# Kernel tuning notes

Hardware: AMD Instinct MI355X
Metric: run time of the kernel (lower is better)

The kernel has to match this reference:

```python
import jax, jax.numpy as jnp
import numpy as np

B, L, D = 2, 2048, 2048
H, KVH = 16, 4
DK = D // H            # 128
REP = H // KVH         # 4
CAP = 50.0


def _rope(x):
    # x: [B, h, L, DK]; rotate-half style RoPE matching the torch module
    half = DK // 2
    inv_freq = 1.0 / (10000.0 ** (jnp.arange(0, DK, 2, dtype=jnp.float32) / DK))
    pos = jnp.arange(x.shape[2], dtype=jnp.float32)
    freqs = pos[:, None] * inv_freq[None, :]          # [L, DK/2]
    cos = jnp.cos(freqs).astype(x.dtype)
    sin = jnp.sin(freqs).astype(x.dtype)
    x1, x2 = x[..., :half], x[..., half:]
    return jnp.concatenate([x1 * cos - x2 * sin, x1 * sin + x2 * cos], axis=-1)


def setup_inputs() -> dict:
    key = jax.random.key(0)
    ks = jax.random.split(key, 7)
    query = jax.random.normal(ks[0], (B, L, D), jnp.float32)
    key_t = jax.random.normal(ks[1], (B, L, D), jnp.float32)
    value = jax.random.normal(ks[2], (B, L, D), jnp.float32)
    mask = jnp.tril(jnp.ones((L, L), dtype=bool))[None, None]  # causal, broadcast over B,H
    s = 1.0 / np.sqrt(D)
    Wq = jax.random.normal(ks[3], (D, D), jnp.float32) * s
    Wk = jax.random.normal(ks[4], (D // REP, D), jnp.float32) * s
    Wv = jax.random.normal(ks[5], (D // REP, D), jnp.float32) * s
    Wo = jax.random.normal(ks[6], (D, D), jnp.float32) * s
    return {"query": query, "key_t": key_t, "value": value, "mask": mask,
            "Wq": Wq, "Wk": Wk, "Wv": Wv, "Wo": Wo}


def reference(query, key_t, value, mask, Wq, Wk, Wv, Wo):
    Lk = key_t.shape[1]
    Q = (query @ Wq.T).reshape(B, L, H, DK).transpose(0, 2, 1, 3)        # [B,H,L,DK]
    K = (key_t @ Wk.T).reshape(B, Lk, KVH, DK).transpose(0, 2, 1, 3)     # [B,KVH,Lk,DK]
    V = (value @ Wv.T).reshape(B, Lk, KVH, DK).transpose(0, 2, 1, 3)
    # repeat_interleave KV heads to match query heads (GQA)
    K = jnp.repeat(K, REP, axis=1)
    V = jnp.repeat(V, REP, axis=1)
    Q = _rope(Q)
    K = _rope(K)
    # module implements "softcap" as a clamp on q/k pre-SDPA
    Q = jnp.clip(Q, -CAP, CAP)
    K = jnp.clip(K, -CAP, CAP)
    scale = 1.0 / np.sqrt(DK)  # SDPA default scaling
    logits = jnp.einsum('bhld,bhkd->bhlk', Q, K) * scale
    neg = jnp.finfo(logits.dtype).min
    logits = logits + jnp.where(mask, jnp.zeros((), logits.dtype), neg)
    attn = jax.nn.softmax(logits, axis=-1)
    out = jnp.einsum('bhlk,bhkd->bhld', attn, V)                         # [B,H,L,DK]
    out = out.transpose(0, 2, 1, 3).reshape(B, L, D)
    return out @ Wo.T
```

## Files before the change

### kernel.cpp

```cpp
#include <hip/hip_runtime.h>

typedef __bf16 bf16;
typedef __bf16 bf16x8 __attribute__((ext_vector_type(8)));
typedef float  f32x4  __attribute__((ext_vector_type(4)));

#define MFMA16(a, b, c) __builtin_amdgcn_mfma_f32_16x16x32_bf16((a), (b), (c), 0, 0, 0)

__device__ inline void gl_lds16(const bf16* g, bf16* l) {
  __builtin_amdgcn_global_load_lds(
      (const __attribute__((address_space(1))) void*)g,
      (__attribute__((address_space(3))) void*)l, 16, 0, 0);
}

__device__ inline bf16x8 cvt8(const float* __restrict__ f) {
  float4 a = *(const float4*)f;
  float4 b = *(const float4*)(f + 4);
  bf16x8 r;
  r[0] = (bf16)a.x; r[1] = (bf16)a.y; r[2] = (bf16)a.z; r[3] = (bf16)a.w;
  r[4] = (bf16)b.x; r[5] = (bf16)b.y; r[6] = (bf16)b.z; r[7] = (bf16)b.w;
  return r;
}

__global__ void cvt_f32_bf16(const float* __restrict__ src, bf16* __restrict__ dst,
                             int n8) {
  int i = blockIdx.x * 256 + threadIdx.x;
  if (i >= n8) return;
  *(bf16x8*)(dst + (size_t)i * 8) = cvt8(src + (size_t)i * 8);
}

__global__ __launch_bounds__(512, 2) void gemm_qkv256(const bf16* __restrict__ qA,
                                                      const bf16* __restrict__ kA,
                                                      const bf16* __restrict__ vA,
                                                      const bf16* __restrict__ W,
                                                      bf16* __restrict__ Qb,
                                                      bf16* __restrict__ Kb,
                                                      bf16* __restrict__ Vb) {
  __shared__ alignas(16) bf16 As[2][32 * 512];
  __shared__ alignas(16) bf16 Bs[2][32 * 512];

  const int tid  = threadIdx.x;
  const int wave = tid >> 6, lane = tid & 63;
  const int wm = wave >> 2, wn = wave & 3;
  const int lr = lane & 15, quad = lane >> 4;
  const int n0 = blockIdx.x * 256, m0 = blockIdx.y * 256;
  const int NS = 32;

  const int range = (n0 < 2048) ? 0 : (n0 < 2560) ? 1 : 2;
  const bf16* Ab = (range == 0) ? qA : (range == 1) ? kA : vA;

  f32x4 vzero = {0.f, 0.f, 0.f, 0.f};
  f32x4 acc[8][4];
#pragma unroll
  for (int mt = 0; mt < 8; ++mt)
#pragma unroll
    for (int nt = 0; nt < 4; ++nt) acc[mt][nt] = vzero;

#define STAGE256(bufi, kk)                                                      \
  do {                                                                          \
    _Pragma("unroll") for (int j = 0; j < 4; ++j) {                             \
      int c = wave * 4 + j;                                                     \
      int mi = c >> 1, sl = c & 1;                                              \
      gl_lds16(Ab + (size_t)(m0 + mi * 16 + lr) * 2048 + (kk) + sl * 32 + quad * 8, \
               &As[bufi][c * 512]);                                             \
      gl_lds16(W + (size_t)(n0 + mi * 16 + lr) * 2048 + (kk) + sl * 32 + quad * 8,  \
               &Bs[bufi][c * 512]);                                             \
    }                                                                           \
  } while (0)

  STAGE256(0, 0);
  int cur = 0;
  for (int t = 0; t < NS; ++t) {
    if (t + 1 < NS) {
      STAGE256(cur ^ 1, (t + 1) * 64);
      asm volatile("s_waitcnt vmcnt(8)" ::: "memory");
    } else {
      asm volatile("s_waitcnt vmcnt(0)" ::: "memory");
    }
    __builtin_amdgcn_s_barrier();

    const bf16* as = As[cur];
    const bf16* bs = Bs[cur];
    bf16x8 af[4], bf0[4], bf1[4];

#pragma unroll
    for (int nt = 0; nt < 4; ++nt)
      bf0[nt] = *(const bf16x8*)(bs + ((wn * 4 + nt) * 2 + 0) * 512 + lane * 8);
#pragma unroll
    for (int mt = 0; mt < 4; ++mt)
      af[mt] = *(const bf16x8*)(as + ((wm * 8 + mt) * 2 + 0) * 512 + lane * 8);
    __builtin_amdgcn_s_setprio(1);
#pragma unroll
    for (int mt = 0; mt < 4; ++mt)
#pragma unroll
      for (int nt = 0; nt < 4; ++nt)
        acc[mt][nt] = MFMA16(af[mt], bf0[nt], acc[mt][nt]);
    __builtin_amdgcn_s_setprio(0);

#pragma unroll
    for (int mt = 0; mt < 4; ++mt)
      af[mt] = *(const bf16x8*)(as + ((wm * 8 + 4 + mt) * 2 + 0) * 512 + lane * 8);
    __builtin_amdgcn_s_setprio(1);
#pragma unroll
    for (int mt = 0; mt < 4; ++mt)
#pragma unroll
      for (int nt = 0; nt < 4; ++nt)
        acc[4 + mt][nt] = MFMA16(af[mt], bf0[nt], acc[4 + mt][nt]);
    __builtin_amdgcn_s_setprio(0);

#pragma unroll
    for (int nt = 0; nt < 4; ++nt)
      bf1[nt] = *(const bf16x8*)(bs + ((wn * 4 + nt) * 2 + 1) * 512 + lane * 8);
#pragma unroll
    for (int mt = 0; mt < 4; ++mt)
      af[mt] = *(const bf16x8*)(as + ((wm * 8 + mt) * 2 + 1) * 512 + lane * 8);
    __builtin_amdgcn_s_setprio(1);
#pragma unroll
    for (int mt = 0; mt < 4; ++mt)
#pragma unroll
      for (int nt = 0; nt < 4; ++nt)
        acc[mt][nt] = MFMA16(af[mt], bf1[nt], acc[mt][nt]);
    __builtin_amdgcn_s_setprio(0);

#pragma unroll
    for (int mt = 0; mt < 4; ++mt)
      af[mt] = *(const bf16x8*)(as + ((wm * 8 + 4 + mt) * 2 + 1) * 512 + lane * 8);
    __builtin_amdgcn_s_setprio(1);
#pragma unroll
    for (int mt = 0; mt < 4; ++mt)
#pragma unroll
      for (int nt = 0; nt < 4; ++nt)
        acc[4 + mt][nt] = MFMA16(af[mt], bf1[nt], acc[4 + mt][nt]);
    __builtin_amdgcn_s_setprio(0);

    __builtin_amdgcn_s_barrier();
    cur ^= 1;
  }
#undef STAGE256

  bf16* Cb = (range == 0) ? Qb : (range == 1) ? Kb : Vb;
  const int ld = (range == 0) ? 2048 : 512;
  const int nb = (range == 0) ? n0 : (range == 1) ? n0 - 2048 : n0 - 2560;
#pragma unroll
  for (int mt = 0; mt < 8; ++mt) {
    int row = m0 + wm * 128 + mt * 16 + quad * 4;
#pragma unroll
    for (int nt = 0; nt < 4; ++nt) {
      int col = nb + wn * 64 + nt * 16 + lr;
#pragma unroll
      for (int e = 0; e < 4; ++e)
        Cb[(size_t)(row + e) * ld + col] = (bf16)acc[mt][nt][e];
    }
  }
}

template <bool OUTF32>
__global__ __launch_bounds__(256) void gemm_bt(const bf16* __restrict__ Ap,
                                               const bf16* __restrict__ W,
                                               void* __restrict__ C0,
                                               int ld0, int M, int N, int K) {
  __shared__ alignas(16) bf16 As[2][16 * 512];
  __shared__ alignas(16) bf16 Bs[2][16 * 512];

  const int tid  = threadIdx.x;
  const int wave = tid >> 6, lane = tid & 63;
  const int wm = wave >> 1, wn = wave & 1;
  const int lr = lane & 15, quad = lane >> 4;
  const int m0 = blockIdx.y * 128, n0 = blockIdx.x * 128;
  const int NS = K >> 6;

  f32x4 vzero = {0.f, 0.f, 0.f, 0.f};
  f32x4 acc[4][4];
#pragma unroll
  for (int mt = 0; mt < 4; ++mt)
#pragma unroll
    for (int nt = 0; nt < 4; ++nt) acc[mt][nt] = vzero;

#define STAGE8(bufi, kk)                                                        \
  do {                                                                          \
    _Pragma("unroll") for (int j = 0; j < 4; ++j) {                             \
      int c = wave * 4 + j;                                                     \
      gl_lds16(W + (size_t)(n0 + (c >> 1) * 16 + lr) * K + (kk) +               \
                   (c & 1) * 32 + quad * 8,                                     \
               &Bs[bufi][c * 512]);                                             \
      gl_lds16(Ap + (size_t)(m0 + (c >> 1) * 16 + lr) * K + (kk) +              \
                   (c & 1) * 32 + quad * 8,                                     \
               &As[bufi][c * 512]);                                             \
    }                                                                           \
  } while (0)

  STAGE8(0, 0);
  int cur = 0;
  for (int t = 0; t < NS; ++t) {
    if (t + 1 < NS) {
      STAGE8(cur ^ 1, (t + 1) * 64);
      asm volatile("s_waitcnt vmcnt(8)" ::: "memory");
    } else {
      asm volatile("s_waitcnt vmcnt(0)" ::: "memory");
    }
    __builtin_amdgcn_s_barrier();
#pragma unroll
    for (int s = 0; s < 2; ++s) {
      bf16x8 af[4], bfg[4];
#pragma unroll
      for (int mt = 0; mt < 4; ++mt)
        af[mt] = *(const bf16x8*)(&As[cur][((wm * 4 + mt) * 2 + s) * 512] + lane * 8);
#pragma unroll
      for (int nt = 0; nt < 4; ++nt)
        bfg[nt] = *(const bf16x8*)(&Bs[cur][((wn * 4 + nt) * 2 + s) * 512] + lane * 8);
      __builtin_amdgcn_s_setprio(1);
#pragma unroll
      for (int mt = 0; mt < 4; ++mt)
#pragma unroll
        for (int nt = 0; nt < 4; ++nt)
          acc[mt][nt] = MFMA16(af[mt], bfg[nt], acc[mt][nt]);
      __builtin_amdgcn_s_setprio(0);
    }
    __builtin_amdgcn_s_barrier();
    cur ^= 1;
  }
#undef STAGE8

#pragma unroll
  for (int mt = 0; mt < 4; ++mt) {
    int row = m0 + wm * 64 + mt * 16 + quad * 4;
#pragma unroll
    for (int nt = 0; nt < 4; ++nt) {
      int col = n0 + wn * 64 + nt * 16 + lr;
#pragma unroll
      for (int e = 0; e < 4; ++e) {
        if (OUTF32)
          ((float*)C0)[(size_t)(row + e) * ld0 + col] = acc[mt][nt][e];
        else
          ((bf16*)C0)[(size_t)(row + e) * ld0 + col] = (bf16)acc[mt][nt][e];
      }
    }
  }
}

__global__ void rope_clip(bf16* __restrict__ X, int heads, float scl) {
  int tpr = heads * 8;
  int idx = blockIdx.x * 256 + threadIdx.x;
  if (idx >= 4096 * tpr) return;
  int r = idx / tpr;
  int rem = idx - r * tpr;
  int h = rem >> 3, j0 = (rem & 7) * 8;
  int l = r & 2047;
  size_t base = (size_t)r * (heads * 128) + h * 128 + j0;
  bf16x8 x1 = *(const bf16x8*)(X + base);
  bf16x8 x2 = *(const bf16x8*)(X + base + 64);
  bf16x8 y1, y2;
#pragma unroll
  for (int t = 0; t < 8; ++t) {
    int j = j0 + t;
    float inv = expf(-(float)j * (9.210340371976184f / 64.0f));
    float s, c;
    sincosf((float)l * inv, &s, &c);
    float a = (float)x1[t], b = (float)x2[t];
    float u = a * c - b * s;
    float v = a * s + b * c;
    y1[t] = (bf16)(fminf(fmaxf(u, -50.f), 50.f) * scl);
    y2[t] = (bf16)(fminf(fmaxf(v, -50.f), 50.f) * scl);
  }
  *(bf16x8*)(X + base)      = y1;
  *(bf16x8*)(X + base + 64) = y2;
}

__global__ void transpose_bf16(const bf16* __restrict__ in, bf16* __restrict__ out,
                               int R, int Cc) {
  __shared__ bf16 t[32][33];
  int b = blockIdx.z;
  const bf16* ip = in + (size_t)b * R * Cc;
  bf16* op = out + (size_t)b * R * Cc;
  int c0 = blockIdx.x * 32, r0 = blockIdx.y * 32;
  int lx = threadIdx.x, ly = threadIdx.y;
#pragma unroll
  for (int i = 0; i < 32; i += 8)
    t[ly + i][lx] = ip[(size_t)(r0 + ly + i) * Cc + c0 + lx];
  __syncthreads();
#pragma unroll
  for (int i = 0; i < 32; i += 8)
    op[(size_t)(c0 + ly + i) * R + r0 + lx] = t[lx][ly + i];
}

__global__ __launch_bounds__(512, 2) void flash(const bf16* __restrict__ Q,
                                                const bf16* __restrict__ Kp,
                                                const bf16* __restrict__ Vt,
                                                bf16* __restrict__ Ctx) {
  __shared__ alignas(16) bf16 Ks[2][16 * 512];
  __shared__ alignas(16) bf16 Vs[2][16 * 512];
  __shared__ alignas(16) bf16 Ps[8][32 * 72];

  const int tid  = threadIdx.x;
  const int wave = tid >> 6, lane = tid & 63;
  const int lr = lane & 15, quad = lane >> 4;
  const int bh = blockIdx.y;
  const int b = bh >> 4, h = bh & 15, hk = h >> 2;
  const int p = blockIdx.x;
  const int qA0 = p * 128, qB0 = (15 - p) * 128;
  const int qbA = qA0 + wave * 16;
  const int qbB = qB0 + wave * 16;
  const int nt = (qB0 + 128) >> 6;

  bf16x8 qfA[4], qfB[4];
  {
    const bf16* qa = Q + ((size_t)(b * 2048 + qbA + lr)) * 2048 + h * 128 + quad * 8;
    const bf16* qbp = Q + ((size_t)(b * 2048 + qbB + lr)) * 2048 + h * 128 + quad * 8;
#pragma unroll
    for (int ks = 0; ks < 4; ++ks) {
      qfA[ks] = *(const bf16x8*)(qa + ks * 32);
      qfB[ks] = *(const bf16x8*)(qbp + ks * 32);
    }
  }

  f32x4 vzero = {0.f, 0.f, 0.f, 0.f};
  f32x4 oA[8], oB[8];
#pragma unroll
  for (int dt = 0; dt < 8; ++dt) { oA[dt] = vzero; oB[dt] = vzero; }
  float flsA[4] = {0.f, 0.f, 0.f, 0.f};
  float flsB[4] = {0.f, 0.f, 0.f, 0.f};

  const bf16* kbase = Kp + (size_t)(b * 2048) * 512 + hk * 128;
  const bf16* vbase = Vt + ((size_t)(b * 512 + hk * 128)) * 2048;

#define STAGE(bufi, kk)                                                         \
  do {                                                                          \
    _Pragma("unroll") for (int j = 0; j < 4; ++j) {                             \
      int c = wave * 4 + j;                                                     \
      if (c < 16) {                                                             \
        gl_lds16(kbase + (size_t)((kk) + (c >> 2) * 16 + lr) * 512 +            \
                     (c & 3) * 32 + quad * 8,                                   \
                 &Ks[bufi][c * 512]);                                           \
      } else {                                                                  \
        int c2 = c - 16;                                                        \
        gl_lds16(vbase + (size_t)((c2 >> 1) * 16 + lr) * 2048 + (kk) +          \
                     (c2 & 1) * 32 + quad * 8,                                  \
                 &Vs[bufi][c2 * 512]);                                          \
      }                                                                         \
    }                                                                           \
  } while (0)

  STAGE(0, 0);
  int cur = 0;

  for (int t = 0; t < nt; ++t) {
    const int k0 = t * 64;
    if (t + 1 < nt) {
      STAGE(cur ^ 1, k0 + 64);
      asm volatile("s_waitcnt vmcnt(4)" ::: "memory");
    } else {
      asm volatile("s_waitcnt vmcnt(0)" ::: "memory");
    }
    __builtin_amdgcn_s_barrier();

    const bf16* ksb = Ks[cur];
    const bf16* vsb = Vs[cur];

    if (k0 <= qbA + 15) {
      f32x4 sA[4], sB[4];
#pragma unroll
      for (int kt = 0; kt < 4; ++kt) { sA[kt] = vzero; sB[kt] = vzero; }
#pragma unroll
      for (int ks = 0; ks < 4; ++ks) {
#pragma unroll
        for (int kt = 0; kt < 4; ++kt) {
          bf16x8 kf = *(const bf16x8*)(ksb + (kt * 4 + ks) * 512 + lane * 8);
          sA[kt] = MFMA16(qfA[ks], kf, sA[kt]);
          sB[kt] = MFMA16(qfB[ks], kf, sB[kt]);
        }
      }
      bf16* pwA = Ps[wave];
      bf16* pwB = Ps[wave] + 16 * 72;
#pragma unroll
      for (int kt = 0; kt < 4; ++kt) {
        int kid = k0 + kt * 16 + lr;
#pragma unroll
        for (int e = 0; e < 4; ++e) {
          int qr = quad * 4 + e;
          float pa = (kid <= qbA + qr) ? __expf(sA[kt][e]) : 0.f;
          float pb = __expf(sB[kt][e]);
          flsA[e] += pa;
          flsB[e] += pb;
          pwA[qr * 72 + kt * 16 + lr] = (bf16)pa;
          pwB[qr * 72 + kt * 16 + lr] = (bf16)pb;
        }
      }
#pragma unroll
      for (int ks2 = 0; ks2 < 2; ++ks2) {
        bf16x8 pfA = *(const bf16x8*)(pwA + (size_t)lr * 72 + ks2 * 32 + quad * 8);
        bf16x8 pfB = *(const bf16x8*)(pwB + (size_t)lr * 72 + ks2 * 32 + quad * 8);
#pragma unroll
        for (int dt = 0; dt < 8; ++dt) {
          bf16x8 vf = *(const bf16x8*)(vsb + (dt * 2 + ks2) * 512 + lane * 8);
          oA[dt] = MFMA16(pfA, vf, oA[dt]);
          oB[dt] = MFMA16(pfB, vf, oB[dt]);
        }
      }
    } else if (k0 <= qbB + 15) {
      f32x4 s[4];
#pragma unroll
      for (int kt = 0; kt < 4; ++kt) s[kt] = vzero;
#pragma unroll
      for (int ks = 0; ks < 4; ++ks) {
#pragma unroll
        for (int kt = 0; kt < 4; ++kt) {
          bf16x8 kf = *(const bf16x8*)(ksb + (kt * 4 + ks) * 512 + lane * 8);
          s[kt] = MFMA16(qfB[ks], kf, s[kt]);
        }
      }
      bf16* pwB = Ps[wave] + 16 * 72;
#pragma unroll
      for (int kt = 0; kt < 4; ++kt) {
        int kid = k0 + kt * 16 + lr;
#pragma unroll
        for (int e = 0; e < 4; ++e) {
          int qr = quad * 4 + e;
          float pb = (kid <= qbB + qr) ? __expf(s[kt][e]) : 0.f;
          flsB[e] += pb;
          pwB[qr * 72 + kt * 16 + lr] = (bf16)pb;
        }
      }
#pragma unroll
      for (int ks2 = 0; ks2 < 2; ++ks2) {
        bf16x8 pf = *(const bf16x8*)(pwB + (size_t)lr * 72 + ks2 * 32 + quad * 8);
#pragma unroll
        for (int dt = 0; dt < 8; ++dt) {
          bf16x8 vf = *(const bf16x8*)(vsb + (dt * 2 + ks2) * 512 + lane * 8);
          oB[dt] = MFMA16(pf, vf, oB[dt]);
        }
      }
    }
    __builtin_amdgcn_s_barrier();
    cur ^= 1;
  }
#undef STAGE

#pragma unroll
  for (int e = 0; e < 4; ++e) {
    float sa = flsA[e];
    sa += __shfl_xor(sa, 1);
    sa += __shfl_xor(sa, 2);
    sa += __shfl_xor(sa, 4);
    sa += __shfl_xor(sa, 8);
    flsA[e] = 1.0f / sa;
    float sb = flsB[e];
    sb += __shfl_xor(sb, 1);
    sb += __shfl_xor(sb, 2);
    sb += __shfl_xor(sb, 4);
    sb += __shfl_xor(sb, 8);
    flsB[e] = 1.0f / sb;
  }

  bf16* ca = Ctx + ((size_t)(b * 2048 + qbA + quad * 4)) * 2048 + h * 128 + lr;
  bf16* cb = Ctx + ((size_t)(b * 2048 + qbB + quad * 4)) * 2048 + h * 128 + lr;
#pragma unroll
  for (int dt = 0; dt < 8; ++dt)
#pragma unroll
    for (int e = 0; e < 4; ++e) {
      ca[(size_t)e * 2048 + dt * 16] = (bf16)(oA[dt][e] * flsA[e]);
      cb[(size_t)e * 2048 + dt * 16] = (bf16)(oB[dt][e] * flsB[e]);
    }
}

extern "C" void kernel_launch(void* const* d_in, const int* in_sizes, int n_in,
                              void* d_out, int out_size, void* d_ws, size_t ws_size,
                              hipStream_t stream) {
  (void)in_sizes; (void)n_in; (void)out_size; (void)ws_size;
  const float* query = (const float*)d_in[0];
  const float* key_t = (const float*)d_in[1];
  const float* value = (const float*)d_in[2];
  const float* Wq = (const float*)d_in[4];
  const float* Wk = (const float*)d_in[5];
  const float* Wv = (const float*)d_in[6];
  const float* Wo = (const float*)d_in[7];

  const size_t MB = 1024ull * 1024ull;
  char* ws  = (char*)d_ws;
  bf16* qbf = (bf16*)(ws);
  bf16* wqb = (bf16*)(ws + 16 * MB);
  bf16* wkb = (bf16*)(ws + 24 * MB);
  bf16* wvb = (bf16*)(ws + 26 * MB);
  bf16* wob = (bf16*)(ws + 28 * MB);
  bf16* Qb  = (bf16*)(ws + 36 * MB);
  bf16* Kb  = (bf16*)(ws + 52 * MB);
  bf16* Vb  = (bf16*)(ws + 56 * MB);
  bf16* Vtb = (bf16*)(ws + 60 * MB);
  bf16* kb16 = (bf16*)(ws + 64 * MB);
  bf16* vb16 = (bf16*)(ws + 80 * MB);
  bf16* Ctx = qbf;

  cvt_f32_bf16<<<4096, 256, 0, stream>>>(query, qbf, 1048576);
  cvt_f32_bf16<<<4096, 256, 0, stream>>>(key_t, kb16, 1048576);
  cvt_f32_bf16<<<4096, 256, 0, stream>>>(value, vb16, 1048576);
  cvt_f32_bf16<<<2048, 256, 0, stream>>>(Wq, wqb, 524288);
  cvt_f32_bf16<<<512, 256, 0, stream>>>(Wk, wkb, 131072);
  cvt_f32_bf16<<<512, 256, 0, stream>>>(Wv, wvb, 131072);
  cvt_f32_bf16<<<2048, 256, 0, stream>>>(Wo, wob, 524288);

  gemm_qkv256<<<dim3(12, 16), 512, 0, stream>>>(qbf, kb16, vb16, wqb, Qb, Kb, Vb);

  rope_clip<<<2048, 256, 0, stream>>>(Qb, 16, 0.08838834764831845f);
  rope_clip<<<512, 256, 0, stream>>>(Kb, 4, 1.0f);

  transpose_bf16<<<dim3(16, 64, 2), dim3(32, 8), 0, stream>>>(Vb, Vtb, 2048, 512);

  flash<<<dim3(8, 32), 512, 0, stream>>>(Qb, Kb, Vtb, Ctx);

  gemm_bt<true><<<dim3(16, 32), 256, 0, stream>>>(
      Ctx, wob, (float*)d_out, 2048, 4096, 2048, 2048);
}
```

Before: 431.5 us.

## Use 256x256 split-K GEMM for output projection with separate reduction

```diff
diff --git a/kernel.cpp b/kernel.cpp
--- a/kernel.cpp
+++ b/kernel.cpp
@@ -28,13 +28,26 @@
   *(bf16x8*)(dst + (size_t)i * 8) = cvt8(src + (size_t)i * 8);
 }
 
-__global__ __launch_bounds__(512, 2) void gemm_qkv256(const bf16* __restrict__ qA,
-                                                      const bf16* __restrict__ kA,
-                                                      const bf16* __restrict__ vA,
-                                                      const bf16* __restrict__ W,
-                                                      bf16* __restrict__ Qb,
-                                                      bf16* __restrict__ Kb,
-                                                      bf16* __restrict__ Vb) {
+__global__ void add_f32(float* __restrict__ dst, const float* __restrict__ src,
+                        int n4) {
+  int i = blockIdx.x * 256 + threadIdx.x;
+  if (i >= n4) return;
+  float4 a = ((const float4*)dst)[i];
+  float4 b = ((const float4*)src)[i];
+  a.x += b.x; a.y += b.y; a.z += b.z; a.w += b.w;
+  ((float4*)dst)[i] = a;
+}
+
+template <int OUTM>
+__global__ __launch_bounds__(512, 2) void gemm256(const bf16* __restrict__ qA,
+                                                  const bf16* __restrict__ kA,
+                                                  const bf16* __restrict__ vA,
+                                                  const bf16* __restrict__ W,
+                                                  bf16* __restrict__ Qb,
+                                                  bf16* __restrict__ Kb,
+                                                  bf16* __restrict__ Vb,
+                                                  float* __restrict__ P0,
+                                                  float* __restrict__ P1) {
   __shared__ alignas(16) bf16 As[2][32 * 512];
   __shared__ alignas(16) bf16 Bs[2][32 * 512];
 
@@ -43,10 +56,17 @@
   const int wm = wave >> 2, wn = wave & 3;
   const int lr = lane & 15, quad = lane >> 4;
   const int n0 = blockIdx.x * 256, m0 = blockIdx.y * 256;
-  const int NS = 32;
-
-  const int range = (n0 < 2048) ? 0 : (n0 < 2560) ? 1 : 2;
-  const bf16* Ab = (range == 0) ? qA : (range == 1) ? kA : vA;
+  const int NS = (OUTM == 0) ? 32 : 16;
+  const int kbase = (OUTM == 0) ? 0 : blockIdx.z * 1024;
+
+  int range = 0;
+  const bf16* Ab;
+  if (OUTM == 0) {
+    range = (n0 < 2048) ? 0 : (n0 < 2560) ? 1 : 2;
+    Ab = (range == 0) ? qA : (range == 1) ? kA : vA;
+  } else {
+    Ab = qA;
+  }
 
   f32x4 vzero = {0.f, 0.f, 0.f, 0.f};
   f32x4 acc[8][4];
@@ -67,11 +87,11 @@
     }                                                                           \
   } while (0)
 
-  STAGE256(0, 0);
+  STAGE256(0, kbase);
   int cur = 0;
   for (int t = 0; t < NS; ++t) {
     if (t + 1 < NS) {
-      STAGE256(cur ^ 1, (t + 1) * 64);
+      STAGE256(cur ^ 1, kbase + (t + 1) * 64);
       asm volatile("s_waitcnt vmcnt(8)" ::: "memory");
     } else {
       asm volatile("s_waitcnt vmcnt(0)" ::: "memory");
@@ -137,101 +157,32 @@
   }
 #undef STAGE256
 
-  bf16* Cb = (range == 0) ? Qb : (range == 1) ? Kb : Vb;
-  const int ld = (range == 0) ? 2048 : 512;
-  const int nb = (range == 0) ? n0 : (range == 1) ? n0 - 2048 : n0 - 2560;
-#pragma unroll
-  for (int mt = 0; mt < 8; ++mt) {
-    int row = m0 + wm * 128 + mt * 16 + quad * 4;
-#pragma unroll
-    for (int nt = 0; nt < 4; ++nt) {
-      int col = nb + wn * 64 + nt * 16 + lr;
-#pragma unroll
-      for (int e = 0; e < 4; ++e)
-        Cb[(size_t)(row + e) * ld + col] = (bf16)acc[mt][nt][e];
-    }
-  }
-}
-
-template <bool OUTF32>
-__global__ __launch_bounds__(256) void gemm_bt(const bf16* __restrict__ Ap,
-                                               const bf16* __restrict__ W,
-                                               void* __restrict__ C0,
-                                               int ld0, int M, int N, int K) {
-  __shared__ alignas(16) bf16 As[2][16 * 512];
-  __shared__ alignas(16) bf16 Bs[2][16 * 512];
-
-  const int tid  = threadIdx.x;
-  const int wave = tid >> 6, lane = tid & 63;
-  const int wm = wave >> 1, wn = wave & 1;
-  const int lr = lane & 15, quad = lane >> 4;
-  const int m0 = blockIdx.y * 128, n0 = blockIdx.x * 128;
-  const int NS = K >> 6;
-
-  f32x4 vzero = {0.f, 0.f, 0.f, 0.f};
-  f32x4 acc[4][4];
-#pragma unroll
-  for (int mt = 0; mt < 4; ++mt)
-#pragma unroll
-    for (int nt = 0; nt < 4; ++nt) acc[mt][nt] = vzero;
-
-#define STAGE8(bufi, kk)                                                        \
-  do {                                                                          \
-    _Pragma("unroll") for (int j = 0; j < 4; ++j) {                             \
-      int c = wave * 4 + j;                                                     \
-      gl_lds16(W + (size_t)(n0 + (c >> 1) * 16 + lr) * K + (kk) +               \
-                   (c & 1) * 32 + quad * 8,                                     \
-               &Bs[bufi][c * 512]);                                             \
-      gl_lds16(Ap + (size_t)(m0 + (c >> 1) * 16 + lr) * K + (kk) +              \
-                   (c & 1) * 32 + quad * 8,                                     \
-               &As[bufi][c * 512]);                                             \
-    }                                                                           \
-  } while (0)
-
-  STAGE8(0, 0);
-  int cur = 0;
-  for (int t = 0; t < NS; ++t) {
-    if (t + 1 < NS) {
-      STAGE8(cur ^ 1, (t + 1) * 64);
-      asm volatile("s_waitcnt vmcnt(8)" ::: "memory");
-    } else {
-      asm volatile("s_waitcnt vmcnt(0)" ::: "memory");
-    }
-    __builtin_amdgcn_s_barrier();
-#pragma unroll
-    for (int s = 0; s < 2; ++s) {
-      bf16x8 af[4], bfg[4];
-#pragma unroll
-      for (int mt = 0; mt < 4; ++mt)
-        af[mt] = *(const bf16x8*)(&As[cur][((wm * 4 + mt) * 2 + s) * 512] + lane * 8);
-#pragma unroll
-      for (int nt = 0; nt < 4; ++nt)
-        bfg[nt] = *(const bf16x8*)(&Bs[cur][((wn * 4 + nt) * 2 + s) * 512] + lane * 8);
-      __builtin_amdgcn_s_setprio(1);
-#pragma unroll
-      for (int mt = 0; mt < 4; ++mt)
-#pragma unroll
-        for (int nt = 0; nt < 4; ++nt)
-          acc[mt][nt] = MFMA16(af[mt], bfg[nt], acc[mt][nt]);
-      __builtin_amdgcn_s_setprio(0);
-    }
-    __builtin_amdgcn_s_barrier();
-    cur ^= 1;
-  }
-#undef STAGE8
-
-#pragma unroll
-  for (int mt = 0; mt < 4; ++mt) {
-    int row = m0 + wm * 64 + mt * 16 + quad * 4;
-#pragma unroll
-    for (int nt = 0; nt < 4; ++nt) {
-      int col = n0 + wn * 64 + nt * 16 + lr;
-#pragma unroll
-      for (int e = 0; e < 4; ++e) {
-        if (OUTF32)
-          ((float*)C0)[(size_t)(row + e) * ld0 + col] = acc[mt][nt][e];
-        else
-          ((bf16*)C0)[(size_t)(row + e) * ld0 + col] = (bf16)acc[mt][nt][e];
+  if (OUTM == 0) {
+    bf16* Cb = (range == 0) ? Qb : (range == 1) ? Kb : Vb;
+    const int ld = (range == 0) ? 2048 : 512;
+    const int nb = (range == 0) ? n0 : (range == 1) ? n0 - 2048 : n0 - 2560;
+#pragma unroll
+    for (int mt = 0; mt < 8; ++mt) {
+      int row = m0 + wm * 128 + mt * 16 + quad * 4;
+#pragma unroll
+      for (int nt = 0; nt < 4; ++nt) {
+        int col = nb + wn * 64 + nt * 16 + lr;
+#pragma unroll
+        for (int e = 0; e < 4; ++e)
+          Cb[(size_t)(row + e) * ld + col] = (bf16)acc[mt][nt][e];
+      }
+    }
+  } else {
+    float* Pb = (blockIdx.z == 0) ? P0 : P1;
+#pragma unroll
+    for (int mt = 0; mt < 8; ++mt) {
+      int row = m0 + wm * 128 + mt * 16 + quad * 4;
+#pragma unroll
+      for (int nt = 0; nt < 4; ++nt) {
+        int col = n0 + wn * 64 + nt * 16 + lr;
+#pragma unroll
+        for (int e = 0; e < 4; ++e)
+          Pb[(size_t)(row + e) * 2048 + col] = acc[mt][nt][e];
       }
     }
   }
@@ -487,6 +438,7 @@
   bf16* kb16 = (bf16*)(ws + 64 * MB);
   bf16* vb16 = (bf16*)(ws + 80 * MB);
   bf16* Ctx = qbf;
+  float* p1 = (float*)(ws + 36 * MB);
 
   cvt_f32_bf16<<<4096, 256, 0, stream>>>(query, qbf, 1048576);
   cvt_f32_bf16<<<4096, 256, 0, stream>>>(key_t, kb16, 1048576);
@@ -496,7 +448,8 @@
   cvt_f32_bf16<<<512, 256, 0, stream>>>(Wv, wvb, 131072);
   cvt_f32_bf16<<<2048, 256, 0, stream>>>(Wo, wob, 524288);
 
-  gemm_qkv256<<<dim3(12, 16), 512, 0, stream>>>(qbf, kb16, vb16, wqb, Qb, Kb, Vb);
+  gemm256<0><<<dim3(12, 16), 512, 0, stream>>>(qbf, kb16, vb16, wqb,
+                                               Qb, Kb, Vb, nullptr, nullptr);
 
   rope_clip<<<2048, 256, 0, stream>>>(Qb, 16, 0.08838834764831845f);
   rope_clip<<<512, 256, 0, stream>>>(Kb, 4, 1.0f);
@@ -505,6 +458,8 @@
 
   flash<<<dim3(8, 32), 512, 0, stream>>>(Qb, Kb, Vtb, Ctx);
 
-  gemm_bt<true><<<dim3(16, 32), 256, 0, stream>>>(
-      Ctx, wob, (float*)d_out, 2048, 4096, 2048, 2048);
-}
+  gemm256<1><<<dim3(8, 16, 2), 512, 0, stream>>>(Ctx, nullptr, nullptr, wob,
+                                                 nullptr, nullptr, nullptr,
+                                                 (float*)d_out, p1);
+  add_f32<<<8192, 256, 0, stream>>>((float*)d_out, p1, 2097152);
+}
```

New measurement: 436.6 us. Within noise of the previous version (+1.2%).
